# Kernel tuning notes

Hardware: AMD Instinct MI355X
Metric: run time of the kernel (lower is better)

Reference implementation:

```python
import jax, jax.numpy as jnp
import numpy as np

N, D, H, E = 50000, 64, 4, 400000
LN_EPS = 1e-5


def setup_inputs() -> dict:
    key = jax.random.key(0)
    ks = jax.random.split(key, 8)
    x = jax.random.normal(ks[0], (N, D), dtype=jnp.float32)
    edge_index = jax.random.randint(ks[1], (2, E), 0, N, dtype=jnp.int64)
    # nn.Linear(dim, dim*heads, bias=False): weight shape (H*D, D)
    W_lin = jax.random.normal(ks[2], (H * D, D), dtype=jnp.float32) * (1.0 / np.sqrt(D))
    attn_src = jax.random.normal(ks[3], (H, D), dtype=jnp.float32) * 0.1
    attn_dst = jax.random.normal(ks[4], (H, D), dtype=jnp.float32) * 0.1
    # nn.Linear(dim*heads, dim): weight (D, H*D), bias (D,)
    W_out = jax.random.normal(ks[5], (D, H * D), dtype=jnp.float32) * (1.0 / np.sqrt(H * D))
    b_out = jnp.zeros((D,), dtype=jnp.float32)
    ln_g = jnp.ones((D,), dtype=jnp.float32)
    ln_b = jnp.zeros((D,), dtype=jnp.float32)
    return {"x": x, "edge_index": edge_index, "W_lin": W_lin,
            "attn_src": attn_src, "attn_dst": attn_dst,
            "W_out": W_out, "b_out": b_out, "ln_g": ln_g, "ln_b": ln_b}


def reference(x, edge_index, W_lin, attn_src, attn_dst, W_out, b_out, ln_g, ln_b):
    n = x.shape[0]
    i, j = edge_index[0], edge_index[1]  # dst, src node ids per edge
    xh = (x @ W_lin.T).reshape(n, H, D)                 # [N,H,D]
    # per-node attention contributions (equivalent to per-edge dot in source)
    s_dst = jnp.einsum('nhd,hd->nh', xh, attn_dst)      # [N,H]
    s_src = jnp.einsum('nhd,hd->nh', xh, attn_src)      # [N,H]
    alpha = jax.nn.leaky_relu(s_dst[i] + s_src[j], 0.2) # [E,H]
    alpha_exp = jnp.exp(alpha)                          # source uses raw exp (no max-shift)
    denom = jax.ops.segment_sum(alpha_exp, i, num_segments=n)  # [N,H]
    attn = alpha_exp / (denom[i] + 1e-9)                # [E,H]
    msg = attn[:, :, None] * xh[j]                      # [E,H,D]
    out = jax.ops.segment_sum(msg, i, num_segments=n)   # [N,H,D]
    out = out.reshape(n, H * D) @ W_out.T + b_out       # [N,D]
    y = jax.nn.elu(out) + x
    mu = jnp.mean(y, axis=-1, keepdims=True)
    var = jnp.mean(jnp.square(y - mu), axis=-1, keepdims=True)
    return (y - mu) * jax.lax.rsqrt(var + LN_EPS) * ln_g + ln_b
```

## Files before the change

kernel.cpp:

```cpp
#include <hip/hip_runtime.h>

#define N_NODES 50000
#define DIM     64
#define HEADS   4
#define NEDGES  400000
#define HD      256
#define MAXDEG  32
#define NPREP   256
#define ZSTRIDE 264

#define USE_DOT2 1

typedef _Float16 half2v __attribute__((ext_vector_type(2)));
typedef _Float16 half4v __attribute__((ext_vector_type(4)));
typedef _Float16 half8v __attribute__((ext_vector_type(8)));
typedef float    f32x4  __attribute__((ext_vector_type(4)));

union EU { int2 i2; half4v h; };
union HU { unsigned int u; half2v h; };

__device__ __forceinline__ half2v h2cast(unsigned int u) { HU c; c.u = u; return c.h; }

#if USE_DOT2
#define DOT2(a, b, c) __builtin_amdgcn_fdot2((a), (b), (c), false)
#else
__device__ __forceinline__ float DOT2(half2v a, half2v b, float c) {
    return fmaf((float)a[1], (float)b[1], fmaf((float)a[0], (float)b[0], c));
}
#endif

__global__ __launch_bounds__(256) void k_prep(
    const float* __restrict__ x,
    const float* __restrict__ W_lin,
    const float* __restrict__ attn_src,
    const float* __restrict__ attn_dst,
    const float* __restrict__ W_out,
    const int* __restrict__ ei,
    _Float16* __restrict__ G2T,
    _Float16* __restrict__ x16,
    float* __restrict__ S,
    int* __restrict__ cnt,
    int* __restrict__ bucketJ)
{
    __shared__ float weffsh[512];
    const int b = blockIdx.x, t = threadIdx.x;

    for (int e = b * 256 + t; e < NEDGES; e += NPREP * 256) {
        const int i = ei[e];
        const int j = ei[NEDGES + e];
        const int slot = atomicAdd(&cnt[i], 1);
        if (slot < MAXDEG) bucketJ[(size_t)i * MAXDEG + slot] = j;
    }

    for (int id = t; id < 512; id += 256) {
        const int sd = id >> 8, rem = id & 255, h = rem >> 6, k = rem & 63;
        const float* av = sd ? attn_dst : attn_src;
        float acc = 0.f;
        for (int d = 0; d < DIM; ++d)
            acc = fmaf(av[h * DIM + d], W_lin[(h * DIM + d) * DIM + k], acc);
        weffsh[id] = acc;
    }

    {
        const int id = b * 256 + t;
        if (id < 64 * 256) {
            const int d = id >> 8, rem = id & 255, m = rem >> 2, h = rem & 3;
            float acc = 0.f;
            for (int k = 0; k < DIM; ++k)
                acc = fmaf(W_lin[(h * DIM + k) * DIM + m],
                           W_out[d * HD + h * DIM + k], acc);
            G2T[d * HD + m * 4 + h] = (_Float16)acc;
        }
    }
    __syncthreads();

    for (int base = b * 32; base < N_NODES; base += NPREP * 32) {
        const int ni = base + (t >> 3);
        if (ni < N_NODES) {
            const int combo = t & 7;
            const float4* xr = (const float4*)(x + (size_t)ni * DIM);
            const float4* wr = (const float4*)(weffsh + combo * DIM);
            float acc = 0.f;
#pragma unroll
            for (int kp = 0; kp < 16; ++kp) {
                const float4 a = xr[kp], bw = wr[kp];
                acc = fmaf(a.x, bw.x, acc);
                acc = fmaf(a.y, bw.y, acc);
                acc = fmaf(a.z, bw.z, acc);
                acc = fmaf(a.w, bw.w, acc);
            }
            S[(size_t)ni * 8 + combo] = acc;
        }
        const size_t e0 = (size_t)base * DIM + (size_t)t * 8;
        if (e0 + 8 <= (size_t)N_NODES * DIM) {
            const float4 u = *(const float4*)(x + e0);
            const float4 v = *(const float4*)(x + e0 + 4);
            half8v hv;
            hv[0]=(_Float16)u.x; hv[1]=(_Float16)u.y; hv[2]=(_Float16)u.z; hv[3]=(_Float16)u.w;
            hv[4]=(_Float16)v.x; hv[5]=(_Float16)v.y; hv[6]=(_Float16)v.z; hv[7]=(_Float16)v.w;
            *(half8v*)(x16 + e0) = hv;
        }
    }
}

__global__ __launch_bounds__(256) void k_ga(
    const int* __restrict__ cnt,
    const int* __restrict__ bucketJ,
    const float* __restrict__ S,
    const _Float16* __restrict__ x16,
    const _Float16* __restrict__ G2T,
    const float* __restrict__ b_out,
    const float* __restrict__ ln_g,
    const float* __restrict__ ln_b,
    float* __restrict__ out)
{
    __shared__ _Float16 znsh[16 * ZSTRIDE];
    __shared__ float ysh[16][65];
    __shared__ int2  esh[16 * 32];

    const int t = threadIdx.x, wv = t >> 6, l = t & 63;
    const int n0 = blockIdx.x * 16;
    const int side = l >> 5, p = l & 31;

    const int4 degv = *(const int4*)(cnt + n0 + wv * 4);
    int degc[4];
    degc[0] = degv.x < MAXDEG ? degv.x : MAXDEG;
    degc[1] = degv.y < MAXDEG ? degv.y : MAXDEG;
    degc[2] = degv.z < MAXDEG ? degv.z : MAXDEG;
    degc[3] = degv.w < MAXDEG ? degv.w : MAXDEG;

    int Jr[4];
#pragma unroll
    for (int r = 0; r < 4; ++r)
        Jr[r] = bucketJ[(unsigned)(n0 + wv * 4 + r) * MAXDEG + p];
#pragma unroll
    for (int r = 0; r < 4; ++r)
        Jr[r] = (p < degc[r]) ? Jr[r] : 0;

    float4 SSr[4], SDr[4];
#pragma unroll
    for (int r = 0; r < 4; ++r)
        SSr[r] = *(const float4*)(S + (unsigned)Jr[r] * 8);
#pragma unroll
    for (int r = 0; r < 4; ++r)
        SDr[r] = *(const float4*)(S + (unsigned)(n0 + wv * 4 + r) * 8 + 4);

#pragma unroll
    for (int r = 0; r < 4; ++r) {
        float u;
        u = SDr[r].x + SSr[r].x; u = u > 0.f ? u : 0.2f * u; const float e0 = __expf(u);
        u = SDr[r].y + SSr[r].y; u = u > 0.f ? u : 0.2f * u; const float e1 = __expf(u);
        u = SDr[r].z + SSr[r].z; u = u > 0.f ? u : 0.2f * u; const float e2 = __expf(u);
        u = SDr[r].w + SSr[r].w; u = u > 0.f ? u : 0.2f * u; const float e3 = __expf(u);
        EU pk;
        pk.h[0] = (_Float16)e0; pk.h[1] = (_Float16)e1;
        pk.h[2] = (_Float16)e2; pk.h[3] = (_Float16)e3;
        int2 ev = pk.i2;
        if (p >= degc[r]) { ev.x = 0; ev.y = 0; }
        if (side == 0) esh[(wv * 4 + r) * 32 + p] = ev;
    }
    __builtin_amdgcn_wave_barrier();

    struct Grp { half2v xv[4]; int2 ee[4]; };
    float za[4], zb[4], dd[4];
    const half2v one2 = h2cast(0x3C003C00u);

    auto stage_group = [&](int r, int s, Grp& g) {
        const int jb = s + side;
#pragma unroll
        for (int q = 0; q < 4; ++q) {
            const int jv = __shfl(Jr[r], jb + 2 * q, 64);
            g.xv[q] = *(const half2v*)(x16 + (unsigned)jv * DIM + (p << 1));
        }
        const int eb = (wv * 4 + r) * 32 + jb;
#pragma unroll
        for (int q = 0; q < 4; ++q)
            g.ee[q] = esh[eb + 2 * q];
    };

    auto consume_group = [&](const Grp& g) {
#pragma unroll
        for (int pp = 0; pp < 2; ++pp) {
            const int2 ea = g.ee[2 * pp], eb2 = g.ee[2 * pp + 1];
            HU xa, xb; xa.h = g.xv[2 * pp]; xb.h = g.xv[2 * pp + 1];
            const unsigned E0 = __builtin_amdgcn_perm(eb2.x, ea.x, 0x05040100u);
            const unsigned E1 = __builtin_amdgcn_perm(eb2.x, ea.x, 0x07060302u);
            const unsigned E2 = __builtin_amdgcn_perm(eb2.y, ea.y, 0x05040100u);
            const unsigned E3 = __builtin_amdgcn_perm(eb2.y, ea.y, 0x07060302u);
            const unsigned XA = __builtin_amdgcn_perm(xb.u, xa.u, 0x05040100u);
            const unsigned XB = __builtin_amdgcn_perm(xb.u, xa.u, 0x07060302u);
            const half2v f0 = h2cast(E0), f1 = h2cast(E1);
            const half2v f2 = h2cast(E2), f3 = h2cast(E3);
            const half2v va = h2cast(XA), vb = h2cast(XB);
            za[0] = DOT2(f0, va, za[0]); za[1] = DOT2(f1, va, za[1]);
            za[2] = DOT2(f2, va, za[2]); za[3] = DOT2(f3, va, za[3]);
            zb[0] = DOT2(f0, vb, zb[0]); zb[1] = DOT2(f1, vb, zb[1]);
            zb[2] = DOT2(f2, vb, zb[2]); zb[3] = DOT2(f3, vb, zb[3]);
            dd[0] = DOT2(f0, one2, dd[0]); dd[1] = DOT2(f1, one2, dd[1]);
            dd[2] = DOT2(f2, one2, dd[2]); dd[3] = DOT2(f3, one2, dd[3]);
        }
    };

    Grp cur, nxt, remb;
    stage_group(0, 0, cur);

#pragma unroll
    for (int r = 0; r < 4; ++r) {
        const bool rem = degc[r] > 8;
        if (rem) stage_group(r, 8, remb);
        if (r < 3) stage_group(r + 1, 0, nxt);

#pragma unroll
        for (int h = 0; h < 4; ++h) { za[h] = 0.f; zb[h] = 0.f; dd[h] = 0.f; }

        consume_group(cur);
        if (rem) {
            consume_group(remb);
            for (int s = 16; s < degc[r]; s += 8) {
                Grp tg;
                stage_group(r, s, tg);
                consume_group(tg);
            }
        }

#pragma unroll
        for (int h = 0; h < 4; ++h) {
            dd[h] += __shfl_xor(dd[h], 32, 64);
            za[h] += __shfl_xor(za[h], 32, 64);
            zb[h] += __shfl_xor(zb[h], 32, 64);
        }
        const float r0 = __builtin_amdgcn_rcpf(dd[0] + 1e-9f);
        const float r1 = __builtin_amdgcn_rcpf(dd[1] + 1e-9f);
        const float r2 = __builtin_amdgcn_rcpf(dd[2] + 1e-9f);
        const float r3 = __builtin_amdgcn_rcpf(dd[3] + 1e-9f);
        if (side == 0) {
            half8v o;
            o[0] = (_Float16)(za[0] * r0); o[1] = (_Float16)(za[1] * r1);
            o[2] = (_Float16)(za[2] * r2); o[3] = (_Float16)(za[3] * r3);
            o[4] = (_Float16)(zb[0] * r0); o[5] = (_Float16)(zb[1] * r1);
            o[6] = (_Float16)(zb[2] * r2); o[7] = (_Float16)(zb[3] * r3);
            *(half8v*)(znsh + (wv * 4 + r) * ZSTRIDE + p * 8) = o;
        }
        cur = nxt;
    }
    __syncthreads();

    const int mrow = l & 15, quad = l >> 4;
    half8v A[8];
    const _Float16* zr = znsh + mrow * ZSTRIDE + quad * 8;
#pragma unroll
    for (int s = 0; s < 8; ++s)
        A[s] = *(const half8v*)(zr + 32 * s);

    const _Float16* gp = G2T + (size_t)(wv * 16 + mrow) * HD + quad * 8;
    f32x4 c = {0.f, 0.f, 0.f, 0.f};
#pragma unroll
    for (int s = 0; s < 8; ++s)
        c = __builtin_amdgcn_mfma_f32_16x16x32_f16(A[s], *(const half8v*)(gp + 32 * s), c, 0, 0, 0);

    const int col = wv * 16 + mrow;
    const float bo = b_out[col];
#pragma unroll
    for (int rho = 0; rho < 4; ++rho) {
        const int nl = quad * 4 + rho;
        const float o = c[rho] + bo;
        const float eo = o > 0.f ? o : expm1f(o);
        ysh[nl][col] = eo + (float)x16[(size_t)(n0 + nl) * DIM + col];
    }
    __syncthreads();

    const float g = ln_g[l], bb = ln_b[l];
#pragma unroll
    for (int r = 0; r < 4; ++r) {
        const int nl = wv * 4 + r;
        const float y = ysh[nl][l];
        float sum = y;
#pragma unroll
        for (int off = 32; off > 0; off >>= 1) sum += __shfl_xor(sum, off, 64);
        const float mu = sum * (1.f / 64.f);
        const float dy = y - mu;
        float vs = dy * dy;
#pragma unroll
        for (int off = 32; off > 0; off >>= 1) vs += __shfl_xor(vs, off, 64);
        const float rr = rsqrtf(vs * (1.f / 64.f) + 1e-5f);
        out[(size_t)(n0 + nl) * DIM + l] = dy * rr * g + bb;
    }
}

extern "C" void kernel_launch(void* const* d_in, const int* in_sizes, int n_in,
                              void* d_out, int out_size, void* d_ws, size_t ws_size,
                              hipStream_t stream)
{
    const float* x        = (const float*)d_in[0];
    const int*   ei       = (const int*)d_in[1];
    const float* W_lin    = (const float*)d_in[2];
    const float* attn_src = (const float*)d_in[3];
    const float* attn_dst = (const float*)d_in[4];
    const float* W_out    = (const float*)d_in[5];
    const float* b_out    = (const float*)d_in[6];
    const float* ln_g     = (const float*)d_in[7];
    const float* ln_b     = (const float*)d_in[8];
    float* out = (float*)d_out;

    char* ws = (char*)d_ws;
    _Float16* x16    = (_Float16*)ws;
    float*    S      = (float*)(x16 + (size_t)N_NODES * DIM);
    _Float16* G2T    = (_Float16*)(S + (size_t)N_NODES * 8);
    int*      cnt    = (int*)(G2T + 64 * HD);
    int*      bucketJ= cnt + N_NODES;

    hipMemsetAsync(cnt, 0, (size_t)N_NODES * sizeof(int), stream);

    k_prep<<<NPREP, 256, 0, stream>>>(x, W_lin, attn_src, attn_dst, W_out, ei,
                                      G2T, x16, S, cnt, bucketJ);

    k_ga<<<N_NODES / 16, 256, 0, stream>>>(cnt, bucketJ, S, x16, G2T,
                                           b_out, ln_g, ln_b, out);
}
```

Baseline: 149.6 us.

## Hoist independent loads, split MFMA accumulators, vectorize LayerNorm epilogue

Issues the bucketJ and destination-score loads before the degree clamping so more memory requests are in flight early. Splits the 8-step MFMA chain into two independent accumulators to shorten the dependency chain. Rewrites the LayerNorm so that 16 lanes share a row, each handling a float4, with one-pass sum and sum-of-squares reductions and vectorized stores. The one-pass variance is less numerically robust, and the padded ysh row stride changes the LDS bank pattern.

```diff
diff --git a/kernel.cpp b/kernel.cpp
--- a/kernel.cpp
+++ b/kernel.cpp
@@ -115,7 +115,7 @@
     float* __restrict__ out)
 {
     __shared__ _Float16 znsh[16 * ZSTRIDE];
-    __shared__ float ysh[16][65];
+    __shared__ float ysh[16][68];
     __shared__ int2  esh[16 * 32];
 
     const int t = threadIdx.x, wv = t >> 6, l = t & 63;
@@ -123,27 +123,31 @@
     const int side = l >> 5, p = l & 31;
 
     const int4 degv = *(const int4*)(cnt + n0 + wv * 4);
+
+    int Jr[4];
+#pragma unroll
+    for (int r = 0; r < 4; ++r)
+        Jr[r] = bucketJ[(unsigned)(n0 + wv * 4 + r) * MAXDEG + p];
+
+    float4 SDr[4];
+#pragma unroll
+    for (int r = 0; r < 4; ++r)
+        SDr[r] = *(const float4*)(S + (unsigned)(n0 + wv * 4 + r) * 8 + 4);
+
     int degc[4];
     degc[0] = degv.x < MAXDEG ? degv.x : MAXDEG;
     degc[1] = degv.y < MAXDEG ? degv.y : MAXDEG;
     degc[2] = degv.z < MAXDEG ? degv.z : MAXDEG;
     degc[3] = degv.w < MAXDEG ? degv.w : MAXDEG;
 
-    int Jr[4];
-#pragma unroll
-    for (int r = 0; r < 4; ++r)
-        Jr[r] = bucketJ[(unsigned)(n0 + wv * 4 + r) * MAXDEG + p];
 #pragma unroll
     for (int r = 0; r < 4; ++r)
         Jr[r] = (p < degc[r]) ? Jr[r] : 0;
 
-    float4 SSr[4], SDr[4];
+    float4 SSr[4];
 #pragma unroll
     for (int r = 0; r < 4; ++r)
         SSr[r] = *(const float4*)(S + (unsigned)Jr[r] * 8);
-#pragma unroll
-    for (int r = 0; r < 4; ++r)
-        SDr[r] = *(const float4*)(S + (unsigned)(n0 + wv * 4 + r) * 8 + 4);
 
 #pragma unroll
     for (int r = 0; r < 4; ++r) {
@@ -253,10 +257,14 @@
         A[s] = *(const half8v*)(zr + 32 * s);
 
     const _Float16* gp = G2T + (size_t)(wv * 16 + mrow) * HD + quad * 8;
-    f32x4 c = {0.f, 0.f, 0.f, 0.f};
-#pragma unroll
-    for (int s = 0; s < 8; ++s)
-        c = __builtin_amdgcn_mfma_f32_16x16x32_f16(A[s], *(const half8v*)(gp + 32 * s), c, 0, 0, 0);
+    f32x4 c0 = {0.f, 0.f, 0.f, 0.f}, c1 = {0.f, 0.f, 0.f, 0.f};
+#pragma unroll
+    for (int s = 0; s < 4; ++s)
+        c0 = __builtin_amdgcn_mfma_f32_16x16x32_f16(A[s], *(const half8v*)(gp + 32 * s), c0, 0, 0, 0);
+#pragma unroll
+    for (int s = 4; s < 8; ++s)
+        c1 = __builtin_amdgcn_mfma_f32_16x16x32_f16(A[s], *(const half8v*)(gp + 32 * s), c1, 0, 0, 0);
+    const f32x4 c = c0 + c1;
 
     const int col = wv * 16 + mrow;
     const float bo = b_out[col];
@@ -269,21 +277,28 @@
     }
     __syncthreads();
 
-    const float g = ln_g[l], bb = ln_b[l];
-#pragma unroll
-    for (int r = 0; r < 4; ++r) {
-        const int nl = wv * 4 + r;
-        const float y = ysh[nl][l];
-        float sum = y;
-#pragma unroll
-        for (int off = 32; off > 0; off >>= 1) sum += __shfl_xor(sum, off, 64);
-        const float mu = sum * (1.f / 64.f);
-        const float dy = y - mu;
-        float vs = dy * dy;
-#pragma unroll
-        for (int off = 32; off > 0; off >>= 1) vs += __shfl_xor(vs, off, 64);
-        const float rr = rsqrtf(vs * (1.f / 64.f) + 1e-5f);
-        out[(size_t)(n0 + nl) * DIM + l] = dy * rr * g + bb;
+    {
+        const int g = l >> 4, c4 = (l & 15) * 4;
+        const int nl = wv * 4 + g;
+        const float4 yv = *(const float4*)(&ysh[nl][c4]);
+        float s1 = (yv.x + yv.y) + (yv.z + yv.w);
+        float s2 = fmaf(yv.x, yv.x, fmaf(yv.y, yv.y, fmaf(yv.z, yv.z, yv.w * yv.w)));
+#pragma unroll
+        for (int off = 8; off > 0; off >>= 1) {
+            s1 += __shfl_xor(s1, off, 64);
+            s2 += __shfl_xor(s2, off, 64);
+        }
+        const float mu = s1 * (1.f / 64.f);
+        const float var = fmaf(-mu, mu, s2 * (1.f / 64.f));
+        const float rr = rsqrtf(var + 1e-5f);
+        const float4 gv = *(const float4*)(ln_g + c4);
+        const float4 bv = *(const float4*)(ln_b + c4);
+        float4 ov;
+        ov.x = (yv.x - mu) * rr * gv.x + bv.x;
+        ov.y = (yv.y - mu) * rr * gv.y + bv.y;
+        ov.z = (yv.z - mu) * rr * gv.z + bv.z;
+        ov.w = (yv.w - mu) * rr * gv.w + bv.w;
+        *(float4*)(out + (size_t)(n0 + nl) * DIM + c4) = ov;
     }
 }
 
```

Result: no change. 147.2 us (-1.6%).
